# Kernel optimization log

Hardware: AMD Instinct MI355X
Metric: run time of the kernel (lower is better)

## Reference

```python
import jax, jax.numpy as jnp
import numpy as np

B = 2
MAX_SEG = 512
HID = 768
N = [256, 1024, 4096, 16384, 65536]          # points per batch, coarse -> fine
C_NAT = [512, 384, 192, 96, 48]              # native feature dims per level
C_FULL = [512, 896, 1088, 1184, 1232]        # after cascading concat (== self.sizes)


def setup_inputs() -> dict:
    key = jax.random.key(0)
    ks = jax.random.split(key, 64)
    inp = {}
    for i in range(5):
        inp[f"x{i}"] = jax.random.normal(ks[i], (B, N[i], C_NAT[i]), jnp.float32)
        inp[f"p2s{i}"] = jax.random.randint(ks[5 + i], (B, N[i]), 0, MAX_SEG)
        inp[f"W{i}"] = jax.random.normal(ks[10 + i], (C_FULL[i], HID), jnp.float32) / np.sqrt(C_FULL[i]).astype(np.float32)
        inp[f"b{i}"] = jnp.zeros((HID,), jnp.float32)
        inp[f"g{i}"] = jnp.ones((HID,), jnp.float32)
        inp[f"be{i}"] = jnp.zeros((HID,), jnp.float32)
    for i in range(1, 5):
        inp[f"inv{i}"] = jax.random.randint(ks[20 + i], (B, N[i]), 0, N[i - 1])
    inp["max_seg"] = MAX_SEG
    return inp


def _scatter_mean(feat, idx, num_seg):
    # feat: [B, N, C], idx: [B, N] -> [B, num_seg, C]; empty segments -> 0 (torch_scatter semantics)
    b, n, c = feat.shape
    flat_idx = (idx + jnp.arange(b, dtype=idx.dtype)[:, None] * num_seg).reshape(-1)
    sums = jax.ops.segment_sum(feat.reshape(b * n, c), flat_idx, num_segments=b * num_seg)
    cnts = jax.ops.segment_sum(jnp.ones((b * n,), feat.dtype), flat_idx, num_segments=b * num_seg)
    return (sums / jnp.maximum(cnts, 1.0)[:, None]).reshape(b, num_seg, c)


def _layer_norm(x, g, be, eps=1e-5):
    m = jnp.mean(x, axis=-1, keepdims=True)
    v = jnp.mean(jnp.square(x - m), axis=-1, keepdims=True)
    return (x - m) * jax.lax.rsqrt(v + eps) * g + be


def reference(x0, x1, x2, x3, x4,
              p2s0, p2s1, p2s2, p2s3, p2s4,
              inv1, inv2, inv3, inv4,
              W0, W1, W2, W3, W4,
              b0, b1, b2, b3, b4,
              g0, g1, g2, g3, g4,
              be0, be1, be2, be3, be4,
              max_seg):
    xs = [x0, x1, x2, x3, x4]
    p2s = [p2s0, p2s1, p2s2, p2s3, p2s4]
    invs = [None, inv1, inv2, inv3, inv4]
    Ws = [W0, W1, W2, W3, W4]
    bs = [b0, b1, b2, b3, b4]
    gs = [g0, g1, g2, g3, g4]
    bes = [be0, be1, be2, be3, be4]

    outs = []
    feat = xs[0]  # coarsest level: [B, N0, 512]
    for i in range(5):
        if i > 0:
            # gather parent feats via inverse map, concat [native, upsampled]
            up = jnp.take_along_axis(feat, invs[i][..., None], axis=1)  # [B, N_i, C_full_{i-1}]
            feat = jnp.concatenate([xs[i], up], axis=-1)                # [B, N_i, C_full_i]
        seg = _scatter_mean(feat, p2s[i], max_seg)                      # [B, max_seg, C_full_i]
        proj = jnp.einsum('bsc,ch->bsh', seg, Ws[i]) + bs[i]
        outs.append(_layer_norm(proj, gs[i], bes[i]))                   # dropout = identity (eval)
    return jnp.stack(outs)  # [5, B, max_seg, HID]
```

## Files before the change

kernel.cpp:

```cpp
#include <hip/hip_runtime.h>
#include <hip/hip_bf16.h>

#define NSEG 512
#define HID 768

typedef __attribute__((ext_vector_type(8))) short s16x8;
typedef __attribute__((ext_vector_type(8))) unsigned short u16x8;
typedef __attribute__((ext_vector_type(4))) unsigned short u16x4;
typedef __attribute__((ext_vector_type(4))) float f32x4;

__device__ __forceinline__ unsigned short f2bf(float x) {
  unsigned u = __builtin_bit_cast(unsigned, x);
  unsigned r = (u + 0x7fff + ((u >> 16) & 1)) >> 16;
  return (unsigned short)r;
}

__device__ __forceinline__ float bf2f(unsigned short h) {
  unsigned u = ((unsigned)h) << 16;
  return __builtin_bit_cast(float, u);
}

__device__ __forceinline__ void gl_lds16(const void* g, void* l) {
  __builtin_amdgcn_global_load_lds(
      (const __attribute__((address_space(1))) unsigned*)g,
      (__attribute__((address_space(3))) unsigned*)l, 16, 0, 0);
}

struct PreArgs {
  const int *inv1, *inv2, *inv3, *inv4;
  int *c20, *c31, *c30, *c42, *c41, *c40;
  const int* p2s[5];
  int* cnt;
};

__device__ __forceinline__ bool lvl_decode(int t, int& lvl, int& u, int& N) {
  if      (t < 512)    { lvl = 0; u = t;          N = 256; }
  else if (t < 2560)   { lvl = 1; u = t - 512;    N = 1024; }
  else if (t < 10752)  { lvl = 2; u = t - 2560;   N = 4096; }
  else if (t < 43520)  { lvl = 3; u = t - 10752;  N = 16384; }
  else if (t < 174592) { lvl = 4; u = t - 43520;  N = 65536; }
  else return false;
  return true;
}

__global__ __launch_bounds__(256)
void pre_k(PreArgs a) {
  int t = blockIdx.x * 256 + threadIdx.x;
  if (t < 8192) {
    int b = (t >= 4096);
    a.c20[t] = a.inv1[b * 1024 + a.inv2[t]];
  } else if (t < 40960) {
    int u = t - 8192;
    int b = (u >= 16384);
    int n2 = a.inv3[u];
    int n1 = a.inv2[b * 4096 + n2]; a.c31[u] = n1;
    a.c30[u] = a.inv1[b * 1024 + n1];
  } else if (t < 172032) {
    int u = t - 40960;
    int b = (u >= 65536);
    int n3 = a.inv4[u];
    int n2 = a.inv3[b * 16384 + n3]; a.c42[u] = n2;
    int n1 = a.inv2[b * 4096 + n2];  a.c41[u] = n1;
    a.c40[u] = a.inv1[b * 1024 + n1];
  } else {
    int u0 = t - 172032;
    int lvl, u, N;
    if (!lvl_decode(u0, lvl, u, N)) return;
    int b = (u >= N);
    atomicAdd(&a.cnt[lvl * 1024 + b * NSEG + a.p2s[lvl][u]], 1);
  }
}

__global__ __launch_bounds__(512)
void scan_k(const int* __restrict__ cnt, int* __restrict__ off, float* __restrict__ scl) {
  __shared__ int sm[NSEG];
  int base = blockIdx.x * NSEG;
  int t = threadIdx.x;
  int v = cnt[base + t];
  sm[t] = v;
  __syncthreads();
  for (int d = 1; d < NSEG; d <<= 1) {
    int u = (t >= d) ? sm[t - d] : 0;
    __syncthreads();
    sm[t] += u;
    __syncthreads();
  }
  off[base + t] = sm[t] - v;
  scl[base + t] = 1.0f / (float)(v > 0 ? v : 1);
}

struct ScArgs { const int* p2s[5]; int* pt[5]; int* cur; const int* off; };

__global__ __launch_bounds__(256)
void scat_all_k(ScArgs a) {
  int t = blockIdx.x * 256 + threadIdx.x;
  int lvl, u, N;
  if (!lvl_decode(t, lvl, u, N)) return;
  int b = (u >= N);
  int n = u - b * N;
  int idx = lvl * 1024 + b * NSEG + a.p2s[lvl][u];
  int pos = a.off[idx] + atomicAdd(&a.cur[idx], 1);
  a.pt[lvl][b * N + pos] = n;
}

struct RedAll {
  const float* x[5][5];
  const int*   ci[5][5];
  int Njl[5][5], CN[5][5], colOFF[5][5];
  int nb[5], N[5], CF[5], nchunk[5];
  const int* pt[5]; const int* cnt[5]; const int* segoff[5];
  float* seg01[2];
  unsigned short* part[5];
};

__global__ __launch_bounds__(256)
void reduce3_k(RedAll A) {
  int gb = blockIdx.x;
  int lvl, lb;
  if      (gb < 1024) { lvl = 0; lb = gb; }
  else if (gb < 2048) { lvl = 1; lb = gb - 1024; }
  else if (gb < 4096) { lvl = 2; lb = gb - 2048; }
  else if (gb < 6144) { lvl = 3; lb = gb - 4096; }
  else                { lvl = 4; lb = gb - 6144; }
  int chunk = lb >> 10;
  int bs    = lb & 1023;
  int b     = bs >> 9;
  int t     = threadIdx.x;
  int m     = A.cnt[lvl][bs];
  int CF    = A.CF[lvl];
  int nb    = A.nb[lvl];
  int N     = A.N[lvl];

  const float* xs[2]; const int* cim[2]; int str[2]; bool val[2];
#pragma unroll
  for (int k = 0; k < 2; k++) {
    int c4 = (t + k * 256) * 4;
    val[k] = c4 < CF;
    xs[k] = nullptr; cim[k] = nullptr; str[k] = 1;
    if (val[k]) {
      int j = 0;
      while (j < nb - 1 && !(c4 >= A.colOFF[lvl][j] && c4 < A.colOFF[lvl][j] + A.CN[lvl][j])) j++;
      xs[k]  = A.x[lvl][j] + (size_t)b * A.Njl[lvl][j] * A.CN[lvl][j] + (c4 - A.colOFF[lvl][j]);
      cim[k] = A.ci[lvl][j] ? (A.ci[lvl][j] + (size_t)b * N) : nullptr;
      str[k] = A.CN[lvl][j];
    }
  }

  bool direct = (lvl <= 1);
  int start = 0, end = m;
  if (!direct) {
    int nch = A.nchunk[lvl];
    int cs = (m + nch - 1) / nch;
    start = chunk * cs;
    end = min(m, start + cs);
  } else if (m == 0) {
    float* so = A.seg01[lvl] + (size_t)bs * CF;
#pragma unroll
    for (int k = 0; k < 2; k++)
      if (val[k]) *(float4*)(so + (t + k * 256) * 4) = make_float4(0.f, 0.f, 0.f, 0.f);
    return;
  }

  float ax[2][4] = {};
  if (start < end) {
    const int* pl = A.pt[lvl] + (size_t)b * N + A.segoff[lvl][bs];
    int p = start;
    for (; p + 8 <= end; p += 8) {
      int n[8];
#pragma unroll
      for (int q = 0; q < 8; q++) n[q] = pl[p + q];
#pragma unroll
      for (int k = 0; k < 2; k++) if (val[k]) {
        int r[8];
#pragma unroll
        for (int q = 0; q < 8; q++) r[q] = cim[k] ? cim[k][n[q]] : n[q];
        float4 v[8];
#pragma unroll
        for (int q = 0; q < 8; q++) v[q] = *(const float4*)(xs[k] + (size_t)r[q] * str[k]);
#pragma unroll
        for (int q = 0; q < 8; q++) {
          ax[k][0] += v[q].x; ax[k][1] += v[q].y; ax[k][2] += v[q].z; ax[k][3] += v[q].w;
        }
      }
    }
    for (; p + 4 <= end; p += 4) {
      int n0 = pl[p], n1 = pl[p + 1], n2 = pl[p + 2], n3 = pl[p + 3];
#pragma unroll
      for (int k = 0; k < 2; k++) if (val[k]) {
        int r0 = cim[k] ? cim[k][n0] : n0;
        int r1 = cim[k] ? cim[k][n1] : n1;
        int r2 = cim[k] ? cim[k][n2] : n2;
        int r3 = cim[k] ? cim[k][n3] : n3;
        float4 v0 = *(const float4*)(xs[k] + (size_t)r0 * str[k]);
        float4 v1 = *(const float4*)(xs[k] + (size_t)r1 * str[k]);
        float4 v2 = *(const float4*)(xs[k] + (size_t)r2 * str[k]);
        float4 v3 = *(const float4*)(xs[k] + (size_t)r3 * str[k]);
        ax[k][0] += (v0.x + v1.x) + (v2.x + v3.x);
        ax[k][1] += (v0.y + v1.y) + (v2.y + v3.y);
        ax[k][2] += (v0.z + v1.z) + (v2.z + v3.z);
        ax[k][3] += (v0.w + v1.w) + (v2.w + v3.w);
      }
    }
    for (; p < end; p++) {
      int n0 = pl[p];
#pragma unroll
      for (int k = 0; k < 2; k++) if (val[k]) {
        int r0 = cim[k] ? cim[k][n0] : n0;
        float4 v0 = *(const float4*)(xs[k] + (size_t)r0 * str[k]);
        ax[k][0] += v0.x; ax[k][1] += v0.y; ax[k][2] += v0.z; ax[k][3] += v0.w;
      }
    }
  }

  if (direct) {
    float* so = A.seg01[lvl] + (size_t)bs * CF;
#pragma unroll
    for (int k = 0; k < 2; k++) if (val[k]) {
      int c4 = (t + k * 256) * 4;
      *(float4*)(so + c4) = make_float4(ax[k][0], ax[k][1], ax[k][2], ax[k][3]);
    }
  } else {
    unsigned short* po = A.part[lvl] + ((size_t)chunk * 1024 + bs) * CF;
#pragma unroll
    for (int k = 0; k < 2; k++) if (val[k]) {
      int c4 = (t + k * 256) * 4;
      u16x4 o = {f2bf(ax[k][0]), f2bf(ax[k][1]), f2bf(ax[k][2]), f2bf(ax[k][3])};
      *(u16x4*)(po + c4) = o;
    }
  }
}

struct CsArgs {
  const float* sg[2];
  const unsigned short* pp[5];
  unsigned short* sb[5];
  const float* scl;
  int CF[5]; int KP[5]; int NC[5];
};

__global__ __launch_bounds__(256)
void conv_seg_k(CsArgs a) {
  int row = blockIdx.x;
  int lvl = row >> 10;
  int rl  = row & 1023;
  int CF = a.CF[lvl], KP = a.KP[lvl];
  int c = threadIdx.x;
  if (c >= (KP >> 3)) return;
  float s = a.scl[row];
  int w = c & 7, blk = c >> 3;
  int k0 = blk * 64 + ((w ^ (rl & 7)) << 3);
  u16x8 o = {0, 0, 0, 0, 0, 0, 0, 0};
  if (k0 < CF) {
    float acc[8] = {};
    if (lvl <= 1) {
      const float* src = a.sg[lvl] + (size_t)rl * CF + k0;
      float4 v0 = *(const float4*)src;
      float4 v1 = *(const float4*)(src + 4);
      acc[0] = v0.x; acc[1] = v0.y; acc[2] = v0.z; acc[3] = v0.w;
      acc[4] = v1.x; acc[5] = v1.y; acc[6] = v1.z; acc[7] = v1.w;
    } else {
      int nc = a.NC[lvl];
      const unsigned short* base = a.pp[lvl] + (size_t)rl * CF + k0;
      for (int n = 0; n < nc; n++) {
        u16x8 v = *(const u16x8*)(base + (size_t)n * 1024 * CF);
#pragma unroll
        for (int e = 0; e < 8; e++) acc[e] += bf2f(v[e]);
      }
    }
#pragma unroll
    for (int e = 0; e < 8; e++) o[e] = f2bf(acc[e] * s);
  }
  *(u16x8*)(a.sb[lvl] + (size_t)rl * KP + c * 8) = o;
}

struct CwArgs { const float* w[5]; unsigned short* wt[5]; int CF[5]; int KP[5]; };

__global__ __launch_bounds__(256)
void conv_wtt_k(CwArgs a) {
  int lvl = blockIdx.y;
  int KP = a.KP[lvl], CF = a.CF[lvl];
  int ntiles = 12 * (KP >> 6);
  int tile = blockIdx.x;
  if (tile >= ntiles) return;
  int kb  = tile / 12;
  int nb0 = tile - kb * 12;
  int t = threadIdx.x;

  __shared__ float lds[64][65];

  const float* wsrc = a.w[lvl];
#pragma unroll
  for (int e = 0; e < 4; e++) {
    int f = e * 256 + t;
    int row = f >> 4;
    int c4  = (f & 15) * 4;
    int k = kb * 64 + row;
    float4 v = make_float4(0.f, 0.f, 0.f, 0.f);
    if (k < CF) v = *(const float4*)(wsrc + (size_t)k * HID + nb0 * 64 + c4);
    lds[row][c4 + 0] = v.x; lds[row][c4 + 1] = v.y;
    lds[row][c4 + 2] = v.z; lds[row][c4 + 3] = v.w;
  }
  __syncthreads();

  unsigned short* wt = a.wt[lvl];
#pragma unroll
  for (int h = 0; h < 2; h++) {
    int idx2 = h * 256 + t;
    int n_loc = idx2 >> 3;
    int w2    = idx2 & 7;
    int kbase = (w2 ^ (n_loc & 7)) << 3;
    u16x8 o;
#pragma unroll
    for (int e = 0; e < 8; e++) o[e] = f2bf(lds[kbase + e][n_loc]);
    int n = nb0 * 64 + n_loc;
    *(u16x8*)(wt + (size_t)n * KP + kb * 64 + w2 * 8) = o;
  }
}

struct G2Args {
  const unsigned short* sb[5];
  const unsigned short* wt[5];
  const float* bias[5];
  float* proj;
  int KP[5];
  int KIT[5];
};

__global__ __launch_bounds__(256)
void gemm2_k(G2Args g) {
  int lvl = blockIdx.z;
  int n0 = blockIdx.x * 64;
  int m0 = blockIdx.y * 128;
  const char* A = (const char*)g.sb[lvl];
  const char* Bw = (const char*)g.wt[lvl];
  int KP = g.KP[lvl];
  int KIT = g.KIT[lvl];

  __shared__ char smem[49152];

  int t = threadIdx.x;
  int lane = t & 63;
  int w = t >> 6;
  int wm = w >> 1, wn = w & 1;

  f32x4 acc[4][2] = {};

  int rowb = t >> 3;
  int colb = (t & 7) * 16;

  auto stg = [&](int buf, int it) {
    char* base = smem + buf * 24576;
#pragma unroll
    for (int j = 0; j < 4; j++) {
      int row = j * 32 + rowb;
      gl_lds16(A + (size_t)(m0 + row) * (KP * 2) + it * 128 + colb,
               base + j * 4096 + t * 16);
    }
#pragma unroll
    for (int j = 0; j < 2; j++) {
      int row = j * 32 + rowb;
      gl_lds16(Bw + (size_t)(n0 + row) * (KP * 2) + it * 128 + colb,
               base + 16384 + j * 4096 + t * 16);
    }
  };

  int r15 = lane & 15, hi = lane >> 4, sx = (lane & 7) << 4;

  stg(0, 0);
  int cur = 0;
  for (int it = 0; it < KIT; ++it) {
    __syncthreads();
    if (it + 1 < KIT) stg(cur ^ 1, it + 1);
    const char* base = smem + cur * 24576;
    s16x8 af[2][4]; s16x8 bf2v[2][2];
#pragma unroll
    for (int s = 0; s < 2; s++) {
      int cb = (s * 64 + hi * 16) ^ sx;
#pragma unroll
      for (int fm = 0; fm < 4; fm++) {
        int row = wm * 64 + fm * 16 + r15;
        af[s][fm] = *(const s16x8*)(base + row * 128 + cb);
      }
#pragma unroll
      for (int fn = 0; fn < 2; fn++) {
        int row = wn * 32 + fn * 16 + r15;
        bf2v[s][fn] = *(const s16x8*)(base + 16384 + row * 128 + cb);
      }
    }
#pragma unroll
    for (int s = 0; s < 2; s++)
#pragma unroll
      for (int fm = 0; fm < 4; fm++)
#pragma unroll
        for (int fn = 0; fn < 2; fn++)
          acc[fm][fn] = __builtin_amdgcn_mfma_f32_16x16x32_bf16(af[s][fm], bf2v[s][fn], acc[fm][fn], 0, 0, 0);
    cur ^= 1;
  }

  const float* bias = g.bias[lvl];
  float* proj = g.proj + ((size_t)lvl * 1024 + m0) * HID;
#pragma unroll
  for (int fm = 0; fm < 4; fm++)
#pragma unroll
    for (int fn = 0; fn < 2; fn++) {
      int col = n0 + wn * 32 + fn * 16 + r15;
      int rb = wm * 64 + fm * 16 + hi * 4;
      float bi = bias[col];
      f32x4 v = acc[fm][fn];
#pragma unroll
      for (int r = 0; r < 4; r++)
        proj[(size_t)(rb + r) * HID + col] = v[r] + bi;
    }
}

struct LnArgs { const float* g[5]; const float* be[5]; };

__global__ __launch_bounds__(256)
void ln_k(LnArgs la, const float* __restrict__ proj, float* __restrict__ out) {
  int row = blockIdx.x;
  int lvl = row >> 10;
  const float* x = proj + (size_t)row * HID;
  int t = threadIdx.x;
  float v0 = x[t], v1 = x[t + 256], v2 = x[t + 512];
  float s = v0 + v1 + v2;
  float q = v0 * v0 + v1 * v1 + v2 * v2;
#pragma unroll
  for (int d = 32; d >= 1; d >>= 1) { s += __shfl_down(s, d); q += __shfl_down(q, d); }
  __shared__ float ps[4], pq[4];
  int w = t >> 6;
  if ((t & 63) == 0) { ps[w] = s; pq[w] = q; }
  __syncthreads();
  float S = ps[0] + ps[1] + ps[2] + ps[3];
  float Q = pq[0] + pq[1] + pq[2] + pq[3];
  float mean = S * (1.0f / HID);
  float var  = Q * (1.0f / HID) - mean * mean;
  float rs   = rsqrtf(var + 1e-5f);
  const float* g  = la.g[lvl];
  const float* be = la.be[lvl];
  float* o = out + (size_t)row * HID;
  o[t]       = (v0 - mean) * rs * g[t]       + be[t];
  o[t + 256] = (v1 - mean) * rs * g[t + 256] + be[t + 256];
  o[t + 512] = (v2 - mean) * rs * g[t + 512] + be[t + 512];
}

extern "C" void kernel_launch(void* const* d_in, const int* in_sizes, int n_in,
                              void* d_out, int out_size, void* d_ws, size_t ws_size,
                              hipStream_t stream) {
  static const int N_[5]  = {256, 1024, 4096, 16384, 65536};
  static const int CN_[5] = {512, 384, 192, 96, 48};
  static const int CF_[5] = {512, 896, 1088, 1184, 1232};
  static const int KP_[5] = {512, 896, 1088, 1216, 1280};
  static const int NC_[5] = {1, 1, 2, 2, 4};

  const float* x[5]; const int* p2s[5]; const float* W[5];
  const float* bias[5]; const float* g[5]; const float* be[5];
  for (int i = 0; i < 5; i++) {
    x[i]    = (const float*)d_in[6 * i + 0];
    p2s[i]  = (const int*)  d_in[6 * i + 1];
    W[i]    = (const float*)d_in[6 * i + 2];
    bias[i] = (const float*)d_in[6 * i + 3];
    g[i]    = (const float*)d_in[6 * i + 4];
    be[i]   = (const float*)d_in[6 * i + 5];
  }
  const int* inv[5] = {nullptr, (const int*)d_in[30], (const int*)d_in[31],
                       (const int*)d_in[32], (const int*)d_in[33]};

  int*   wsi = (int*)d_ws;
  float* wsf = (float*)d_ws;
  unsigned short* wsu = (unsigned short*)d_ws;

  const int CNT = 0, CUR = 5120, OFS = 10240, SCL = 15360;
  static const int PT[5]   = {20480, 20992, 23040, 31232, 64000};
  const int CI20 = 195072, CI31 = 203264, CI30 = 236032;
  const int CI42 = 268800, CI41 = 399872, CI40 = 530944;
  static const int SG01[2] = {662016, 1186304};
  static const int PPu[5]  = {0, 0, 4207616, 6435840, 8860672};
  static const int SBu[5]  = {13906944, 14431232, 15348736, 16462848, 17708032};
  static const int WTu[5]  = {1324032, 1717248, 2405376, 3240960, 4174848};
  const int PROJ = 2578944;

  hipMemsetAsync(wsi + CNT, 0, (size_t)10240 * 4, stream);

  PreArgs pa{inv[1], inv[2], inv[3], inv[4],
             wsi + CI20, wsi + CI31, wsi + CI30, wsi + CI42, wsi + CI41, wsi + CI40,
             {}, wsi + CNT};
  for (int i = 0; i < 5; i++) pa.p2s[i] = p2s[i];
  pre_k<<<1354, 256, 0, stream>>>(pa);

  scan_k<<<10, 512, 0, stream>>>(wsi + CNT, wsi + OFS, wsf + SCL);

  ScArgs sc{};
  for (int i = 0; i < 5; i++) { sc.p2s[i] = p2s[i]; sc.pt[i] = wsi + PT[i]; }
  sc.cur = wsi + CUR; sc.off = wsi + OFS;
  scat_all_k<<<682, 256, 0, stream>>>(sc);

  const int* cimap[5][5] = {};
  cimap[1][0] = inv[1];
  cimap[2][1] = inv[2]; cimap[2][0] = wsi + CI20;
  cimap[3][2] = inv[3]; cimap[3][1] = wsi + CI31; cimap[3][0] = wsi + CI30;
  cimap[4][3] = inv[4]; cimap[4][2] = wsi + CI42; cimap[4][1] = wsi + CI41; cimap[4][0] = wsi + CI40;

  int offs[5][5] = {};
  for (int i = 1; i < 5; i++)
    for (int j = i - 1; j >= 0; j--) offs[i][j] = CN_[i] + offs[i - 1][j];

  RedAll ra{};
  for (int i = 0; i < 5; i++) {
    int d = 0;
    for (int j = i; j >= 0; j--) {
      ra.x[i][d]      = x[j];
      ra.ci[i][d]     = (j == i) ? nullptr : cimap[i][j];
      ra.Njl[i][d]    = N_[j];
      ra.CN[i][d]     = CN_[j];
      ra.colOFF[i][d] = offs[i][j];
      d++;
    }
    ra.nb[i] = d; ra.N[i] = N_[i]; ra.CF[i] = CF_[i]; ra.nchunk[i] = NC_[i];
    ra.pt[i] = wsi + PT[i]; ra.cnt[i] = wsi + CNT + i * 1024;
    ra.segoff[i] = wsi + OFS + i * 1024;
    ra.part[i] = (i >= 2) ? (wsu + PPu[i]) : nullptr;
  }
  ra.seg01[0] = wsf + SG01[0]; ra.seg01[1] = wsf + SG01[1];
  reduce3_k<<<10240, 256, 0, stream>>>(ra);

  CsArgs ca{};
  ca.sg[0] = wsf + SG01[0]; ca.sg[1] = wsf + SG01[1];
  for (int i = 0; i < 5; i++) {
    ca.pp[i] = (i >= 2) ? (wsu + PPu[i]) : nullptr;
    ca.sb[i] = wsu + SBu[i];
    ca.CF[i] = CF_[i]; ca.KP[i] = KP_[i]; ca.NC[i] = NC_[i];
  }
  ca.scl = wsf + SCL;
  conv_seg_k<<<5120, 256, 0, stream>>>(ca);

  CwArgs cw{};
  for (int i = 0; i < 5; i++) { cw.w[i] = W[i]; cw.wt[i] = wsu + WTu[i]; cw.CF[i] = CF_[i]; cw.KP[i] = KP_[i]; }
  conv_wtt_k<<<dim3(240, 5), 256, 0, stream>>>(cw);

  G2Args ga{};
  for (int i = 0; i < 5; i++) {
    ga.sb[i] = wsu + SBu[i]; ga.wt[i] = wsu + WTu[i]; ga.bias[i] = bias[i];
    ga.KP[i] = KP_[i]; ga.KIT[i] = KP_[i] >> 6;
  }
  ga.proj = wsf + PROJ;
  gemm2_k<<<dim3(12, 8, 5), 256, 0, stream>>>(ga);

  LnArgs la{};
  for (int i = 0; i < 5; i++) { la.g[i] = g[i]; la.be[i] = be[i]; }
  ln_k<<<5120, 256, 0, stream>>>(la, wsf + PROJ, (float*)d_out);
}
```

Measured before the change: 171.4 us.

## Split level 3/4 segment reductions across waves by chunk and column groups

Levels 0-2 keep the old block-per-segment path, minus the 4-wide tail loop. Levels 3 and 4 are restructured. Each block now covers one segment and one column group, and each of its four waves reduces a separate point chunk, with one float4 column per lane. The grid grows from 10240 to 22528 blocks. The goal is more parallelism and memory-level concurrency for the large fine levels, at the cost of idle lanes in partial column groups and more block launches.

```diff
diff --git a/kernel.cpp b/kernel.cpp
--- a/kernel.cpp
+++ b/kernel.cpp
@@ -116,117 +116,165 @@
 __global__ __launch_bounds__(256)
 void reduce3_k(RedAll A) {
   int gb = blockIdx.x;
-  int lvl, lb;
-  if      (gb < 1024) { lvl = 0; lb = gb; }
-  else if (gb < 2048) { lvl = 1; lb = gb - 1024; }
-  else if (gb < 4096) { lvl = 2; lb = gb - 2048; }
-  else if (gb < 6144) { lvl = 3; lb = gb - 4096; }
-  else                { lvl = 4; lb = gb - 6144; }
-  int chunk = lb >> 10;
-  int bs    = lb & 1023;
-  int b     = bs >> 9;
-  int t     = threadIdx.x;
-  int m     = A.cnt[lvl][bs];
-  int CF    = A.CF[lvl];
-  int nb    = A.nb[lvl];
-  int N     = A.N[lvl];
-
-  const float* xs[2]; const int* cim[2]; int str[2]; bool val[2];
-#pragma unroll
-  for (int k = 0; k < 2; k++) {
-    int c4 = (t + k * 256) * 4;
-    val[k] = c4 < CF;
-    xs[k] = nullptr; cim[k] = nullptr; str[k] = 1;
-    if (val[k]) {
-      int j = 0;
-      while (j < nb - 1 && !(c4 >= A.colOFF[lvl][j] && c4 < A.colOFF[lvl][j] + A.CN[lvl][j])) j++;
-      xs[k]  = A.x[lvl][j] + (size_t)b * A.Njl[lvl][j] * A.CN[lvl][j] + (c4 - A.colOFF[lvl][j]);
-      cim[k] = A.ci[lvl][j] ? (A.ci[lvl][j] + (size_t)b * N) : nullptr;
-      str[k] = A.CN[lvl][j];
-    }
-  }
-
-  bool direct = (lvl <= 1);
-  int start = 0, end = m;
-  if (!direct) {
-    int nch = A.nchunk[lvl];
-    int cs = (m + nch - 1) / nch;
-    start = chunk * cs;
-    end = min(m, start + cs);
-  } else if (m == 0) {
-    float* so = A.seg01[lvl] + (size_t)bs * CF;
-#pragma unroll
-    for (int k = 0; k < 2; k++)
-      if (val[k]) *(float4*)(so + (t + k * 256) * 4) = make_float4(0.f, 0.f, 0.f, 0.f);
+
+  if (gb < 4096) {
+    int lvl, lb;
+    if      (gb < 1024) { lvl = 0; lb = gb; }
+    else if (gb < 2048) { lvl = 1; lb = gb - 1024; }
+    else                { lvl = 2; lb = gb - 2048; }
+    int chunk = lb >> 10;
+    int bs    = lb & 1023;
+    int b     = bs >> 9;
+    int t     = threadIdx.x;
+    int m     = A.cnt[lvl][bs];
+    int CF    = A.CF[lvl];
+    int nb    = A.nb[lvl];
+    int N     = A.N[lvl];
+
+    const float* xs[2]; const int* cim[2]; int str[2]; bool val[2];
+#pragma unroll
+    for (int k = 0; k < 2; k++) {
+      int c4 = (t + k * 256) * 4;
+      val[k] = c4 < CF;
+      xs[k] = nullptr; cim[k] = nullptr; str[k] = 1;
+      if (val[k]) {
+        int j = 0;
+        while (j < nb - 1 && !(c4 >= A.colOFF[lvl][j] && c4 < A.colOFF[lvl][j] + A.CN[lvl][j])) j++;
+        xs[k]  = A.x[lvl][j] + (size_t)b * A.Njl[lvl][j] * A.CN[lvl][j] + (c4 - A.colOFF[lvl][j]);
+        cim[k] = A.ci[lvl][j] ? (A.ci[lvl][j] + (size_t)b * N) : nullptr;
+        str[k] = A.CN[lvl][j];
+      }
+    }
+
+    bool direct = (lvl <= 1);
+    int start = 0, end = m;
+    if (!direct) {
+      int nch = A.nchunk[lvl];
+      int cs = (m + nch - 1) / nch;
+      start = chunk * cs;
+      end = min(m, start + cs);
+    } else if (m == 0) {
+      float* so = A.seg01[lvl] + (size_t)bs * CF;
+#pragma unroll
+      for (int k = 0; k < 2; k++)
+        if (val[k]) *(float4*)(so + (t + k * 256) * 4) = make_float4(0.f, 0.f, 0.f, 0.f);
+      return;
+    }
+
+    float ax[2][4] = {};
+    if (start < end) {
+      const int* pl = A.pt[lvl] + (size_t)b * N + A.segoff[lvl][bs];
+      int p = start;
+      for (; p + 8 <= end; p += 8) {
+        int n[8];
+#pragma unroll
+        for (int q = 0; q < 8; q++) n[q] = pl[p + q];
+#pragma unroll
+        for (int k = 0; k < 2; k++) if (val[k]) {
+          int r[8];
+#pragma unroll
+          for (int q = 0; q < 8; q++) r[q] = cim[k] ? cim[k][n[q]] : n[q];
+          float4 v[8];
+#pragma unroll
+          for (int q = 0; q < 8; q++) v[q] = *(const float4*)(xs[k] + (size_t)r[q] * str[k]);
+#pragma unroll
+          for (int q = 0; q < 8; q++) {
+            ax[k][0] += v[q].x; ax[k][1] += v[q].y; ax[k][2] += v[q].z; ax[k][3] += v[q].w;
+          }
+        }
+      }
+      for (; p < end; p++) {
+        int n0 = pl[p];
+#pragma unroll
+        for (int k = 0; k < 2; k++) if (val[k]) {
+          int r0 = cim[k] ? cim[k][n0] : n0;
+          float4 v0 = *(const float4*)(xs[k] + (size_t)r0 * str[k]);
+          ax[k][0] += v0.x; ax[k][1] += v0.y; ax[k][2] += v0.z; ax[k][3] += v0.w;
+        }
+      }
+    }
+
+    if (direct) {
+      float* so = A.seg01[lvl] + (size_t)bs * CF;
+#pragma unroll
+      for (int k = 0; k < 2; k++) if (val[k]) {
+        int c4 = (t + k * 256) * 4;
+        *(float4*)(so + c4) = make_float4(ax[k][0], ax[k][1], ax[k][2], ax[k][3]);
+      }
+    } else {
+      unsigned short* po = A.part[lvl] + ((size_t)chunk * 1024 + bs) * CF;
+#pragma unroll
+      for (int k = 0; k < 2; k++) if (val[k]) {
+        int c4 = (t + k * 256) * 4;
+        u16x4 o = {f2bf(ax[k][0]), f2bf(ax[k][1]), f2bf(ax[k][2]), f2bf(ax[k][3])};
+        *(u16x4*)(po + c4) = o;
+      }
+    }
     return;
   }
 
-  float ax[2][4] = {};
-  if (start < end) {
+  int lvl, bs, gbase, gcnt;
+  if (gb < 5120)       { lvl = 3; bs = gb - 4096; gbase = 0; gcnt = 24; }
+  else if (gb < 6144)  { lvl = 4; bs = gb - 5120; gbase = 0; gcnt = 12; }
+  else if (gb < 14336) { int l = gb - 6144;  lvl = 3; bs = l >> 3; gbase = 24 + 34 * (l & 7); gcnt = 34; }
+  else                 { int l = gb - 14336; lvl = 4; bs = l >> 3; gbase = 12 + 37 * (l & 7); gcnt = 37; }
+
+  int wave = threadIdx.x >> 6;
+  int lane = threadIdx.x & 63;
+  int NC = A.nchunk[lvl];
+  if (wave >= NC) return;
+  int m  = A.cnt[lvl][bs];
+  int b  = bs >> 9;
+  int N  = A.N[lvl];
+  int CF = A.CF[lvl];
+
+  bool val = lane < gcnt;
+  int c4 = (gbase + lane) * 4;
+  const float* xs = nullptr; const int* cim = nullptr; int str = 1;
+  if (val) {
+    int nb = A.nb[lvl];
+    int j = 0;
+    while (j < nb - 1 && !(c4 >= A.colOFF[lvl][j] && c4 < A.colOFF[lvl][j] + A.CN[lvl][j])) j++;
+    xs  = A.x[lvl][j] + (size_t)b * A.Njl[lvl][j] * A.CN[lvl][j] + (c4 - A.colOFF[lvl][j]);
+    cim = A.ci[lvl][j] ? (A.ci[lvl][j] + (size_t)b * N) : nullptr;
+    str = A.CN[lvl][j];
+  }
+
+  int cs = (m + NC - 1) / NC;
+  int start = wave * cs;
+  int end = min(m, start + cs);
+
+  float a0 = 0.f, a1 = 0.f, a2 = 0.f, a3 = 0.f;
+  if (val && start < end) {
     const int* pl = A.pt[lvl] + (size_t)b * N + A.segoff[lvl][bs];
     int p = start;
     for (; p + 8 <= end; p += 8) {
       int n[8];
 #pragma unroll
       for (int q = 0; q < 8; q++) n[q] = pl[p + q];
-#pragma unroll
-      for (int k = 0; k < 2; k++) if (val[k]) {
-        int r[8];
-#pragma unroll
-        for (int q = 0; q < 8; q++) r[q] = cim[k] ? cim[k][n[q]] : n[q];
-        float4 v[8];
-#pragma unroll
-        for (int q = 0; q < 8; q++) v[q] = *(const float4*)(xs[k] + (size_t)r[q] * str[k]);
-#pragma unroll
-        for (int q = 0; q < 8; q++) {
-          ax[k][0] += v[q].x; ax[k][1] += v[q].y; ax[k][2] += v[q].z; ax[k][3] += v[q].w;
-        }
-      }
-    }
-    for (; p + 4 <= end; p += 4) {
-      int n0 = pl[p], n1 = pl[p + 1], n2 = pl[p + 2], n3 = pl[p + 3];
-#pragma unroll
-      for (int k = 0; k < 2; k++) if (val[k]) {
-        int r0 = cim[k] ? cim[k][n0] : n0;
-        int r1 = cim[k] ? cim[k][n1] : n1;
-        int r2 = cim[k] ? cim[k][n2] : n2;
-        int r3 = cim[k] ? cim[k][n3] : n3;
-        float4 v0 = *(const float4*)(xs[k] + (size_t)r0 * str[k]);
-        float4 v1 = *(const float4*)(xs[k] + (size_t)r1 * str[k]);
-        float4 v2 = *(const float4*)(xs[k] + (size_t)r2 * str[k]);
-        float4 v3 = *(const float4*)(xs[k] + (size_t)r3 * str[k]);
-        ax[k][0] += (v0.x + v1.x) + (v2.x + v3.x);
-        ax[k][1] += (v0.y + v1.y) + (v2.y + v3.y);
-        ax[k][2] += (v0.z + v1.z) + (v2.z + v3.z);
-        ax[k][3] += (v0.w + v1.w) + (v2.w + v3.w);
+      int r[8];
+#pragma unroll
+      for (int q = 0; q < 8; q++) r[q] = cim ? cim[n[q]] : n[q];
+      float4 v[8];
+#pragma unroll
+      for (int q = 0; q < 8; q++) v[q] = *(const float4*)(xs + (size_t)r[q] * str);
+#pragma unroll
+      for (int q = 0; q < 8; q++) {
+        a0 += v[q].x; a1 += v[q].y; a2 += v[q].z; a3 += v[q].w;
       }
     }
     for (; p < end; p++) {
       int n0 = pl[p];
-#pragma unroll
-      for (int k = 0; k < 2; k++) if (val[k]) {
-        int r0 = cim[k] ? cim[k][n0] : n0;
-        float4 v0 = *(const float4*)(xs[k] + (size_t)r0 * str[k]);
-        ax[k][0] += v0.x; ax[k][1] += v0.y; ax[k][2] += v0.z; ax[k][3] += v0.w;
-      }
-    }
-  }
-
-  if (direct) {
-    float* so = A.seg01[lvl] + (size_t)bs * CF;
-#pragma unroll
-    for (int k = 0; k < 2; k++) if (val[k]) {
-      int c4 = (t + k * 256) * 4;
-      *(float4*)(so + c4) = make_float4(ax[k][0], ax[k][1], ax[k][2], ax[k][3]);
-    }
-  } else {
-    unsigned short* po = A.part[lvl] + ((size_t)chunk * 1024 + bs) * CF;
-#pragma unroll
-    for (int k = 0; k < 2; k++) if (val[k]) {
-      int c4 = (t + k * 256) * 4;
-      u16x4 o = {f2bf(ax[k][0]), f2bf(ax[k][1]), f2bf(ax[k][2]), f2bf(ax[k][3])};
-      *(u16x4*)(po + c4) = o;
-    }
+      int r0 = cim ? cim[n0] : n0;
+      float4 v0 = *(const float4*)(xs + (size_t)r0 * str);
+      a0 += v0.x; a1 += v0.y; a2 += v0.z; a3 += v0.w;
+    }
+  }
+
+  if (val) {
+    unsigned short* po = A.part[lvl] + ((size_t)wave * 1024 + bs) * CF + c4;
+    u16x4 o = {f2bf(a0), f2bf(a1), f2bf(a2), f2bf(a3)};
+    *(u16x4*)po = o;
   }
 }
 
@@ -521,7 +569,7 @@
     ra.part[i] = (i >= 2) ? (wsu + PPu[i]) : nullptr;
   }
   ra.seg01[0] = wsf + SG01[0]; ra.seg01[1] = wsf + SG01[1];
-  reduce3_k<<<10240, 256, 0, stream>>>(ra);
+  reduce3_k<<<22528, 256, 0, stream>>>(ra);
 
   CsArgs ca{};
   ca.sg[0] = wsf + SG01[0]; ca.sg[1] = wsf + SG01[1];
```

Measured after the change: 204.3 us. 19.2% more time.

## Write levels 0-1 bf16 segments directly from reduce and merge conversion kernels

Applied to the files above, without the earlier changes.

For levels 0 and 1, the reduce kernel now applies the mean scale and writes swizzled bf16 rows straight into the GEMM input buffer. This removes the fp32 intermediate segment buffer and its re-read. The segment-conversion and weight-transpose kernels are combined into one launch, which saves a kernel launch and lets the two kinds of work overlap. The 4-wide tail loop is dropped and the workspace offsets for the transposed weights are relocated, so there is a risk of buffer aliasing if the new offsets overlap other regions.

```diff
diff --git a/kernel.cpp b/kernel.cpp
--- a/kernel.cpp
+++ b/kernel.cpp
@@ -109,7 +109,8 @@
   int Njl[5][5], CN[5][5], colOFF[5][5];
   int nb[5], N[5], CF[5], nchunk[5];
   const int* pt[5]; const int* cnt[5]; const int* segoff[5];
-  float* seg01[2];
+  unsigned short* sb01[2];
+  const float* scl;
   unsigned short* part[5];
 };
 
@@ -153,12 +154,6 @@
     int cs = (m + nch - 1) / nch;
     start = chunk * cs;
     end = min(m, start + cs);
-  } else if (m == 0) {
-    float* so = A.seg01[lvl] + (size_t)bs * CF;
-#pragma unroll
-    for (int k = 0; k < 2; k++)
-      if (val[k]) *(float4*)(so + (t + k * 256) * 4) = make_float4(0.f, 0.f, 0.f, 0.f);
-    return;
   }
 
   float ax[2][4] = {};
@@ -183,24 +178,6 @@
         }
       }
     }
-    for (; p + 4 <= end; p += 4) {
-      int n0 = pl[p], n1 = pl[p + 1], n2 = pl[p + 2], n3 = pl[p + 3];
-#pragma unroll
-      for (int k = 0; k < 2; k++) if (val[k]) {
-        int r0 = cim[k] ? cim[k][n0] : n0;
-        int r1 = cim[k] ? cim[k][n1] : n1;
-        int r2 = cim[k] ? cim[k][n2] : n2;
-        int r3 = cim[k] ? cim[k][n3] : n3;
-        float4 v0 = *(const float4*)(xs[k] + (size_t)r0 * str[k]);
-        float4 v1 = *(const float4*)(xs[k] + (size_t)r1 * str[k]);
-        float4 v2 = *(const float4*)(xs[k] + (size_t)r2 * str[k]);
-        float4 v3 = *(const float4*)(xs[k] + (size_t)r3 * str[k]);
-        ax[k][0] += (v0.x + v1.x) + (v2.x + v3.x);
-        ax[k][1] += (v0.y + v1.y) + (v2.y + v3.y);
-        ax[k][2] += (v0.z + v1.z) + (v2.z + v3.z);
-        ax[k][3] += (v0.w + v1.w) + (v2.w + v3.w);
-      }
-    }
     for (; p < end; p++) {
       int n0 = pl[p];
 #pragma unroll
@@ -213,11 +190,16 @@
   }
 
   if (direct) {
-    float* so = A.seg01[lvl] + (size_t)bs * CF;
+    float s = A.scl[lvl * 1024 + bs];
+    unsigned short* sbp = A.sb01[lvl];
 #pragma unroll
     for (int k = 0; k < 2; k++) if (val[k]) {
-      int c4 = (t + k * 256) * 4;
-      *(float4*)(so + c4) = make_float4(ax[k][0], ax[k][1], ax[k][2], ax[k][3]);
+      int g = t + k * 256;
+      int co = g >> 1, half = g & 1;
+      int kb = co >> 3, w0 = co & 7;
+      int c_st = kb * 8 + (w0 ^ (bs & 7));
+      u16x4 o = {f2bf(ax[k][0] * s), f2bf(ax[k][1] * s), f2bf(ax[k][2] * s), f2bf(ax[k][3] * s)};
+      *(u16x4*)(sbp + (size_t)bs * CF + c_st * 8 + half * 4) = o;
     }
   } else {
     unsigned short* po = A.part[lvl] + ((size_t)chunk * 1024 + bs) * CF;
@@ -230,35 +212,33 @@
   }
 }
 
-struct CsArgs {
-  const float* sg[2];
+struct CvArgs {
   const unsigned short* pp[5];
   unsigned short* sb[5];
   const float* scl;
   int CF[5]; int KP[5]; int NC[5];
+  const float* w[5];
+  unsigned short* wt[5];
 };
 
 __global__ __launch_bounds__(256)
-void conv_seg_k(CsArgs a) {
-  int row = blockIdx.x;
-  int lvl = row >> 10;
-  int rl  = row & 1023;
-  int CF = a.CF[lvl], KP = a.KP[lvl];
-  int c = threadIdx.x;
-  if (c >= (KP >> 3)) return;
-  float s = a.scl[row];
-  int w = c & 7, blk = c >> 3;
-  int k0 = blk * 64 + ((w ^ (rl & 7)) << 3);
-  u16x8 o = {0, 0, 0, 0, 0, 0, 0, 0};
-  if (k0 < CF) {
-    float acc[8] = {};
-    if (lvl <= 1) {
-      const float* src = a.sg[lvl] + (size_t)rl * CF + k0;
-      float4 v0 = *(const float4*)src;
-      float4 v1 = *(const float4*)(src + 4);
-      acc[0] = v0.x; acc[1] = v0.y; acc[2] = v0.z; acc[3] = v0.w;
-      acc[4] = v1.x; acc[5] = v1.y; acc[6] = v1.z; acc[7] = v1.w;
-    } else {
+void conv_all_k(CvArgs a) {
+  __shared__ float lds[64][65];
+  int blk = blockIdx.x;
+  int t = threadIdx.x;
+
+  if (blk < 3072) {
+    int lvl = 2 + (blk >> 10);
+    int rl  = blk & 1023;
+    int CF = a.CF[lvl], KP = a.KP[lvl];
+    int c = t;
+    if (c >= (KP >> 3)) return;
+    float s = a.scl[lvl * 1024 + rl];
+    int w = c & 7, kb = c >> 3;
+    int k0 = kb * 64 + ((w ^ (rl & 7)) << 3);
+    u16x8 o = {0, 0, 0, 0, 0, 0, 0, 0};
+    if (k0 < CF) {
+      float acc[8] = {};
       int nc = a.NC[lvl];
       const unsigned short* base = a.pp[lvl] + (size_t)rl * CF + k0;
       for (int n = 0; n < nc; n++) {
@@ -266,27 +246,21 @@
 #pragma unroll
         for (int e = 0; e < 8; e++) acc[e] += bf2f(v[e]);
       }
-    }
-#pragma unroll
-    for (int e = 0; e < 8; e++) o[e] = f2bf(acc[e] * s);
-  }
-  *(u16x8*)(a.sb[lvl] + (size_t)rl * KP + c * 8) = o;
-}
-
-struct CwArgs { const float* w[5]; unsigned short* wt[5]; int CF[5]; int KP[5]; };
-
-__global__ __launch_bounds__(256)
-void conv_wtt_k(CwArgs a) {
-  int lvl = blockIdx.y;
+#pragma unroll
+      for (int e = 0; e < 8; e++) o[e] = f2bf(acc[e] * s);
+    }
+    *(u16x8*)(a.sb[lvl] + (size_t)rl * KP + c * 8) = o;
+    return;
+  }
+
+  int idx = blk - 3072;
+  int lvl = idx / 240;
+  int tile = idx - lvl * 240;
   int KP = a.KP[lvl], CF = a.CF[lvl];
   int ntiles = 12 * (KP >> 6);
-  int tile = blockIdx.x;
   if (tile >= ntiles) return;
   int kb  = tile / 12;
   int nb0 = tile - kb * 12;
-  int t = threadIdx.x;
-
-  __shared__ float lds[64][65];
 
   const float* wsrc = a.w[lvl];
 #pragma unroll
@@ -473,10 +447,9 @@
   static const int PT[5]   = {20480, 20992, 23040, 31232, 64000};
   const int CI20 = 195072, CI31 = 203264, CI30 = 236032;
   const int CI42 = 268800, CI41 = 399872, CI40 = 530944;
-  static const int SG01[2] = {662016, 1186304};
   static const int PPu[5]  = {0, 0, 4207616, 6435840, 8860672};
   static const int SBu[5]  = {13906944, 14431232, 15348736, 16462848, 17708032};
-  static const int WTu[5]  = {1324032, 1717248, 2405376, 3240960, 4174848};
+  static const int WTu[5]  = {40960, 434176, 1122304, 1957888, 2891776};
   const int PROJ = 2578944;
 
   hipMemsetAsync(wsi + CNT, 0, (size_t)10240 * 4, stream);
@@ -520,22 +493,19 @@
     ra.segoff[i] = wsi + OFS + i * 1024;
     ra.part[i] = (i >= 2) ? (wsu + PPu[i]) : nullptr;
   }
-  ra.seg01[0] = wsf + SG01[0]; ra.seg01[1] = wsf + SG01[1];
+  ra.sb01[0] = wsu + SBu[0]; ra.sb01[1] = wsu + SBu[1];
+  ra.scl = wsf + SCL;
   reduce3_k<<<10240, 256, 0, stream>>>(ra);
 
-  CsArgs ca{};
-  ca.sg[0] = wsf + SG01[0]; ca.sg[1] = wsf + SG01[1];
+  CvArgs cv{};
   for (int i = 0; i < 5; i++) {
-    ca.pp[i] = (i >= 2) ? (wsu + PPu[i]) : nullptr;
-    ca.sb[i] = wsu + SBu[i];
-    ca.CF[i] = CF_[i]; ca.KP[i] = KP_[i]; ca.NC[i] = NC_[i];
-  }
-  ca.scl = wsf + SCL;
-  conv_seg_k<<<5120, 256, 0, stream>>>(ca);
-
-  CwArgs cw{};
-  for (int i = 0; i < 5; i++) { cw.w[i] = W[i]; cw.wt[i] = wsu + WTu[i]; cw.CF[i] = CF_[i]; cw.KP[i] = KP_[i]; }
-  conv_wtt_k<<<dim3(240, 5), 256, 0, stream>>>(cw);
+    cv.pp[i] = (i >= 2) ? (wsu + PPu[i]) : nullptr;
+    cv.sb[i] = wsu + SBu[i];
+    cv.CF[i] = CF_[i]; cv.KP[i] = KP_[i]; cv.NC[i] = NC_[i];
+    cv.w[i] = W[i]; cv.wt[i] = wsu + WTu[i];
+  }
+  cv.scl = wsf + SCL;
+  conv_all_k<<<4272, 256, 0, stream>>>(cv);
 
   G2Args ga{};
   for (int i = 0; i < 5; i++) {
```

Result: no change. 171.7 us (+0.2%).
